# Kernel optimization log

Hardware: AMD Instinct MI355X
Metric: run time of the kernel (lower is better)

## Reference

```python
import jax, jax.numpy as jnp
import numpy as np

HEADS = 16
DIM_HEAD = 64
SCALE = DIM_HEAD ** -0.5
NEG = -jnp.finfo(jnp.float32).max


def setup_inputs() -> dict:
    key = jax.random.key(0)
    ks = jax.random.split(key, 5)
    b, n, dim = 2, 2048, 1024
    inner = HEADS * DIM_HEAD
    s = dim ** -0.5  # keep pre-softmax logits well-scaled
    return {
        "x": jax.random.normal(ks[0], (b, n, dim), jnp.float32),
        "mask": jnp.ones((b, n), dtype=bool),
        "Wq": jax.random.normal(ks[1], (dim, inner), jnp.float32) * s,
        "Wk": jax.random.normal(ks[2], (dim, inner), jnp.float32) * s,
        "Wv": jax.random.normal(ks[3], (dim, inner), jnp.float32) * s,
        "Wo": jax.random.normal(ks[4], (inner, dim), jnp.float32) * s,
    }


def reference(x, mask, Wq, Wk, Wv, Wo):
    b, n, _ = x.shape
    # projections, split heads: b n (h d) -> b h n d
    def split(t):
        return t.reshape(b, n, HEADS, DIM_HEAD).transpose(0, 2, 1, 3)
    q = split(x @ Wq)
    k = split(x @ Wk)
    v = split(x @ Wv)
    dots = jnp.einsum("bhid,bhjd->bhij", q, k) * SCALE  # [b,h,n,n]
    # padding mask: b j -> b 1 1 j
    dots = jnp.where(mask[:, None, None, :], dots, NEG)
    # causal mask (strict upper triangle masked)
    causal = jnp.triu(jnp.ones((n, n), dtype=bool), k=1)
    dots = jnp.where(causal, NEG, dots)
    attn = jax.nn.softmax(dots, axis=-1)
    out = jnp.einsum("bhij,bhjd->bhid", attn, v)
    out = out.transpose(0, 2, 1, 3).reshape(b, n, HEADS * DIM_HEAD)
    return out @ Wo
```

## Files before the change

kernel.cpp:

```cpp
#include <hip/hip_runtime.h>
#include <hip/hip_bf16.h>

typedef __bf16 bf16x8 __attribute__((ext_vector_type(8)));
typedef float f32x4 __attribute__((ext_vector_type(4)));
typedef unsigned short u16;
typedef unsigned int u32;

#define MFMA16(A, B, C) __builtin_amdgcn_mfma_f32_16x16x32_bf16((A), (B), (C), 0, 0, 0)

#define BATCH 2
#define SEQ   2048
#define DIM   1024
#define NHEAD 16
#define DHEAD 64
#define MROWS 4096
#define Q_SCALE 0.18033688f

__device__ __forceinline__ u16 f2bf(float f) {
    unsigned int u = __float_as_uint(f);
    u += 0x7fff + ((u >> 16) & 1);
    return (u16)(u >> 16);
}

__device__ __forceinline__ u32 pk2bf(float a, float b) {
    __hip_bfloat162 c = __float22bfloat162_rn(float2{a, b});
    u32 r;
    __builtin_memcpy(&r, &c, 4);
    return r;
}

__device__ __forceinline__ void glds16(const u16* g, u16* l) {
    __builtin_amdgcn_global_load_lds(
        (const __attribute__((address_space(1))) u32*)g,
        (__attribute__((address_space(3))) u32*)l, 16, 0, 0);
}

__global__ __launch_bounds__(256) void prep(const float* __restrict__ x,
                                            const float* __restrict__ wq,
                                            const float* __restrict__ wk,
                                            const float* __restrict__ wv,
                                            const float* __restrict__ wo,
                                            u16* __restrict__ xb,
                                            u16* __restrict__ wt) {
    const int b = blockIdx.x;
    const int t = threadIdx.x;
    if (b < 2048) {
        int i = (b * 256 + t) * 8;
        float4 a = *(const float4*)(x + i);
        float4 c = *(const float4*)(x + i + 4);
        u16 o[8] = {f2bf(a.x), f2bf(a.y), f2bf(a.z), f2bf(a.w),
                    f2bf(c.x), f2bf(c.y), f2bf(c.z), f2bf(c.w)};
        *(uint4*)(xb + i) = *(uint4*)o;
        return;
    }
    __shared__ u16 tile[64][65];
    const int bb = b - 2048;
    const int z = bb >> 8, rem = bb & 255;
    const float* W = (z == 0) ? wq : (z == 1) ? wk : (z == 2) ? wv : wo;
    u16* out = wt + (size_t)z * DIM * DIM;
    int k0 = (rem & 15) * 64;
    int n0 = (rem >> 4) * 64;
    int c = t & 63, r4 = t >> 6;
#pragma unroll
    for (int i = 0; i < 16; i++) {
        int row = i * 4 + r4;
        tile[row][c] = f2bf(W[(size_t)(k0 + row) * DIM + n0 + c]);
    }
    __syncthreads();
#pragma unroll
    for (int i = 0; i < 16; i++) {
        int row = i * 4 + r4;
        out[(size_t)(n0 + row) * DIM + k0 + c] = tile[c][row];
    }
}

__global__ __launch_bounds__(256) void gemm_qkv(const u16* __restrict__ xb,
                                                const u16* __restrict__ wt,
                                                u16* __restrict__ qb,
                                                u16* __restrict__ kb,
                                                u16* __restrict__ vtb) {
    __shared__ __align__(16) u16 SMEM[17408];
    u16* const As = SMEM;
    u16* const Bs = SMEM + 8192;

    const int z = blockIdx.z;
    const u16* Apan = xb;
    const u16* Bpan = wt + (size_t)z * DIM * DIM;
    const int m0 = blockIdx.y * 128, n0 = blockIdx.x * 128;
    const int t = threadIdx.x, w = t >> 6, lane = t & 63;
    const int quad = lane >> 4, l16 = lane & 15;
    const int wm = (w >> 1) * 64, wn = (w & 1) * 64;
    const int srow = lane >> 3;
    const int scol = ((lane & 7) ^ srow) * 8;
    const int fo0 = ((quad) ^ (l16 & 7)) * 8;
    const int fo1 = ((4 + quad) ^ (l16 & 7)) * 8;

    f32x4 acc[4][4] = {};
    for (int k0 = 0; k0 < DIM; k0 += 64) {
        if (k0) __syncthreads();
#pragma unroll
        for (int j = 0; j < 4; j++) {
            int rb = w * 32 + j * 8;
            glds16(Apan + (size_t)(m0 + rb + srow) * DIM + k0 + scol, &As[rb * 64]);
            glds16(Bpan + (size_t)(n0 + rb + srow) * DIM + k0 + scol, &Bs[rb * 64]);
        }
        __syncthreads();

        bf16x8 af[4][2], bfr[4][2];
#pragma unroll
        for (int mt = 0; mt < 4; mt++) {
            const u16* p = &As[(wm + mt * 16 + l16) * 64];
            af[mt][0] = *(const bf16x8*)(p + fo0);
            af[mt][1] = *(const bf16x8*)(p + fo1);
        }
#pragma unroll
        for (int nt = 0; nt < 4; nt++) {
            const u16* p = &Bs[(wn + nt * 16 + l16) * 64];
            bfr[nt][0] = *(const bf16x8*)(p + fo0);
            bfr[nt][1] = *(const bf16x8*)(p + fo1);
        }
#pragma unroll
        for (int mt = 0; mt < 4; mt++)
#pragma unroll
            for (int nt = 0; nt < 4; nt++) {
                acc[mt][nt] = MFMA16(af[mt][0], bfr[nt][0], acc[mt][nt]);
                acc[mt][nt] = MFMA16(af[mt][1], bfr[nt][1], acc[mt][nt]);
            }
    }

    const int bi = m0 >> 11;
    if (z < 2) {
        const float sc = (z == 0) ? Q_SCALE : 1.0f;
        u16* dst = (z == 0) ? qb : kb;
#pragma unroll
        for (int mt = 0; mt < 4; mt++)
#pragma unroll
            for (int nt = 0; nt < 4; nt++)
#pragma unroll
                for (int r = 0; r < 4; r++) {
                    int gm = m0 + wm + mt * 16 + quad * 4 + r;
                    int gc = n0 + wn + nt * 16 + l16;
                    int si = gm & (SEQ - 1);
                    int h = gc >> 6, d = gc & 63;
                    dst[(((size_t)bi * NHEAD + h) * SEQ + si) * DHEAD + d] =
                        f2bf(acc[mt][nt][r] * sc);
                }
    } else {
        __syncthreads();
        u16* T = SMEM;
#pragma unroll
        for (int mt = 0; mt < 4; mt++)
#pragma unroll
            for (int nt = 0; nt < 4; nt++)
#pragma unroll
                for (int r = 0; r < 4; r++)
                    T[(wn + nt * 16 + l16) * 136 + wm + mt * 16 + quad * 4 + r] =
                        f2bf(acc[mt][nt][r]);
        __syncthreads();
        const int row = t >> 1;
        const int half = (t & 1) * 64;
        const int gc = n0 + row;
        const int h = gc >> 6, d = gc & 63;
        const size_t gb = (((size_t)bi * NHEAD + h) * DHEAD + d) * SEQ +
                          (m0 & (SEQ - 1)) + half;
#pragma unroll
        for (int i = 0; i < 8; i++)
            *(uint4*)&vtb[gb + i * 8] = *(const uint4*)&T[row * 136 + half + i * 8];
    }
}

#define LPAD 72
#define OSTR 68
__global__ __launch_bounds__(256) void attn(const u16* __restrict__ qg,
                                            const u16* __restrict__ kg,
                                            const u16* __restrict__ vtg,
                                            u16* __restrict__ og) {
    __shared__ __align__(16) u16 Ks[2][64 * LPAD];
    __shared__ __align__(16) u16 Vs[2][64 * LPAD];
    __shared__ __align__(16) u16 Ps[64 * LPAD];
    __shared__ __align__(16) float Os[64 * OSTR];
    __shared__ float Ls[64];

    const int linear = blockIdx.x;
    const int kidx = linear >> 3;
    const int bh = (linear & 7) * 4 + (kidx >> 4);
    const int px = kidx & 15;
    const int t = threadIdx.x, w = t >> 6, lane = t & 63;
    const int quad = lane >> 4, l16 = lane & 15;
    const int wq32 = (w >> 1) * 32, kh = w & 1, kh32 = kh * 32;
    const int srow = t >> 2, sc16 = (t & 3) * 16;
    const size_t qkbase = (size_t)bh * SEQ;
    const size_t vbase = (size_t)bh * DHEAD;
    const int bi = bh >> 4, hh = bh & 15;

    uint4 pk0, pk1, pv0, pv1;
    auto prefetch = [&](int j0) {
        const u16* kp = &kg[(qkbase + j0 + srow) * DHEAD + sc16];
        pk0 = *(const uint4*)kp;
        pk1 = *(const uint4*)(kp + 8);
        const u16* vp = &vtg[(vbase + srow) * SEQ + j0 + sc16];
        pv0 = *(const uint4*)vp;
        pv1 = *(const uint4*)(vp + 8);
    };

    for (int half = 0; half < 2; half++) {
        const int qt = half ? (31 - px) : px;
        const int q0 = qt * 64;
        const int last = qt;
        const int rowmin = q0 + wq32;

        bf16x8 bq[2][2];
#pragma unroll
        for (int ct = 0; ct < 2; ct++) {
            const u16* qp = qg + (qkbase + q0 + wq32 + ct * 16 + l16) * DHEAD;
            bq[ct][0] = *(const bf16x8*)(qp + quad * 8);
            bq[ct][1] = *(const bf16x8*)(qp + 32 + quad * 8);
        }

        f32x4 accO[4][2] = {};
        float l_part[2] = {0.f, 0.f};

        prefetch(0);
        __syncthreads();

        for (int jt = 0; jt <= last; jt++) {
            const int buf = jt & 1;
            u16* ksb = &Ks[buf][0];
            u16* vsb = &Vs[buf][0];
            *(uint4*)&ksb[srow * LPAD + sc16] = pk0;
            *(uint4*)&ksb[srow * LPAD + sc16 + 8] = pk1;
            *(uint4*)&vsb[srow * LPAD + sc16] = pv0;
            *(uint4*)&vsb[srow * LPAD + sc16 + 8] = pv1;
            __syncthreads();
            if (jt < last) prefetch((jt + 1) * 64);

            const int j0 = jt * 64;
            if (j0 + kh32 > rowmin + 31) continue;
            const bool need_mask = (j0 + kh32 + 31 > rowmin);

            bf16x8 ak[2][2];
#pragma unroll
            for (int nt = 0; nt < 2; nt++) {
                const u16* kr = &ksb[(kh32 + nt * 16 + l16) * LPAD];
                ak[nt][0] = *(const bf16x8*)(kr + quad * 8);
                ak[nt][1] = *(const bf16x8*)(kr + 32 + quad * 8);
            }
            f32x4 s[2][2];
            __builtin_amdgcn_s_setprio(1);
#pragma unroll
            for (int nt = 0; nt < 2; nt++)
#pragma unroll
                for (int ct = 0; ct < 2; ct++) {
                    f32x4 aa = {};
                    aa = MFMA16(ak[nt][0], bq[ct][0], aa);
                    aa = MFMA16(ak[nt][1], bq[ct][1], aa);
                    s[nt][ct] = aa;
                }
            __builtin_amdgcn_s_setprio(0);

            if (need_mask) {
#pragma unroll
                for (int ct = 0; ct < 2; ct++) {
                    int qv = q0 + wq32 + ct * 16 + l16;
#pragma unroll
                    for (int nt = 0; nt < 2; nt++) {
                        int kb = j0 + kh32 + nt * 16 + quad * 4;
                        float p[4];
#pragma unroll
                        for (int r = 0; r < 4; r++)
                            p[r] = (kb + r > qv) ? 0.f
                                 : __builtin_amdgcn_exp2f(s[nt][ct][r]);
                        l_part[ct] += (p[0] + p[1]) + (p[2] + p[3]);
                        uint2 pkd = {pk2bf(p[0], p[1]), pk2bf(p[2], p[3])};
                        *(uint2*)&Ps[(wq32 + ct * 16 + l16) * LPAD + kh32 +
                                     nt * 16 + quad * 4] = pkd;
                    }
                }
            } else {
#pragma unroll
                for (int ct = 0; ct < 2; ct++)
#pragma unroll
                    for (int nt = 0; nt < 2; nt++) {
                        float p[4];
#pragma unroll
                        for (int r = 0; r < 4; r++)
                            p[r] = __builtin_amdgcn_exp2f(s[nt][ct][r]);
                        l_part[ct] += (p[0] + p[1]) + (p[2] + p[3]);
                        uint2 pkd = {pk2bf(p[0], p[1]), pk2bf(p[2], p[3])};
                        *(uint2*)&Ps[(wq32 + ct * 16 + l16) * LPAD + kh32 +
                                     nt * 16 + quad * 4] = pkd;
                    }
            }

            bf16x8 bp[2];
#pragma unroll
            for (int ct = 0; ct < 2; ct++)
                bp[ct] = *(const bf16x8*)&Ps[(wq32 + ct * 16 + l16) * LPAD +
                                             kh32 + quad * 8];
            __builtin_amdgcn_s_setprio(1);
#pragma unroll
            for (int mt = 0; mt < 4; mt++) {
                bf16x8 av = *(const bf16x8*)&vsb[(mt * 16 + l16) * LPAD +
                                                 kh32 + quad * 8];
#pragma unroll
                for (int ct = 0; ct < 2; ct++)
                    accO[mt][ct] = MFMA16(av, bp[ct], accO[mt][ct]);
            }
            __builtin_amdgcn_s_setprio(0);
        }

        float l2[2];
#pragma unroll
        for (int ct = 0; ct < 2; ct++) {
            float l = l_part[ct];
            l += __shfl_xor(l, 16);
            l += __shfl_xor(l, 32);
            l2[ct] = l;
        }
        if (kh == 1) {
            if (quad == 0) {
                Ls[wq32 + l16] = l2[0];
                Ls[wq32 + 16 + l16] = l2[1];
            }
#pragma unroll
            for (int mt = 0; mt < 4; mt++)
#pragma unroll
                for (int ct = 0; ct < 2; ct++)
                    *(float4*)&Os[(wq32 + ct * 16 + l16) * OSTR + mt * 16 +
                                  quad * 4] =
                        float4{accO[mt][ct][0], accO[mt][ct][1],
                               accO[mt][ct][2], accO[mt][ct][3]};
        }
        __syncthreads();
        if (kh == 0) {
#pragma unroll
            for (int ct = 0; ct < 2; ct++) {
                int q = q0 + wq32 + ct * 16 + l16;
                float rl = 1.0f / (l2[ct] + Ls[wq32 + ct * 16 + l16]);
                size_t obase = ((size_t)bi * SEQ + q) * DIM + hh * DHEAD;
#pragma unroll
                for (int mt = 0; mt < 4; mt++) {
                    float4 o = *(float4*)&Os[(wq32 + ct * 16 + l16) * OSTR +
                                             mt * 16 + quad * 4];
                    float v0 = (accO[mt][ct][0] + o.x) * rl;
                    float v1 = (accO[mt][ct][1] + o.y) * rl;
                    float v2 = (accO[mt][ct][2] + o.z) * rl;
                    float v3 = (accO[mt][ct][3] + o.w) * rl;
                    uint2 pkd = {pk2bf(v0, v1), pk2bf(v2, v3)};
                    *(uint2*)&og[obase + mt * 16 + quad * 4] = pkd;
                }
            }
        }
    }
}

__global__ __launch_bounds__(256) void gemm_out(const u16* __restrict__ ob,
                                                const u16* __restrict__ wot,
                                                float* __restrict__ out) {
    __shared__ __align__(16) u16 As[64 * 64];
    __shared__ __align__(16) u16 Bs[128 * 64];
    const int m0 = blockIdx.y * 64, n0 = blockIdx.x * 128;
    const int t = threadIdx.x, w = t >> 6, lane = t & 63;
    const int quad = lane >> 4, l16 = lane & 15;
    const int wm = (w >> 1) * 32, wn = (w & 1) * 64;
    const int srow = lane >> 3;
    const int scol = ((lane & 7) ^ srow) * 8;
    const int fo0 = ((quad) ^ (l16 & 7)) * 8;
    const int fo1 = ((4 + quad) ^ (l16 & 7)) * 8;

    f32x4 acc[2][4] = {};
    for (int k0 = 0; k0 < DIM; k0 += 64) {
        if (k0) __syncthreads();
#pragma unroll
        for (int j = 0; j < 2; j++) {
            int rb = w * 16 + j * 8;
            glds16(&ob[(size_t)(m0 + rb + srow) * DIM + k0 + scol], &As[rb * 64]);
        }
#pragma unroll
        for (int j = 0; j < 4; j++) {
            int rb = w * 32 + j * 8;
            glds16(&wot[(size_t)(n0 + rb + srow) * DIM + k0 + scol], &Bs[rb * 64]);
        }
        __syncthreads();

        bf16x8 af[2][2], bfr[4][2];
#pragma unroll
        for (int mt = 0; mt < 2; mt++) {
            const u16* p = &As[(wm + mt * 16 + l16) * 64];
            af[mt][0] = *(const bf16x8*)(p + fo0);
            af[mt][1] = *(const bf16x8*)(p + fo1);
        }
#pragma unroll
        for (int nt = 0; nt < 4; nt++) {
            const u16* p = &Bs[(wn + nt * 16 + l16) * 64];
            bfr[nt][0] = *(const bf16x8*)(p + fo0);
            bfr[nt][1] = *(const bf16x8*)(p + fo1);
        }
#pragma unroll
        for (int mt = 0; mt < 2; mt++)
#pragma unroll
            for (int nt = 0; nt < 4; nt++) {
                acc[mt][nt] = MFMA16(af[mt][0], bfr[nt][0], acc[mt][nt]);
                acc[mt][nt] = MFMA16(af[mt][1], bfr[nt][1], acc[mt][nt]);
            }
    }
#pragma unroll
    for (int mt = 0; mt < 2; mt++)
#pragma unroll
        for (int nt = 0; nt < 4; nt++)
#pragma unroll
            for (int r = 0; r < 4; r++) {
                int gm = m0 + wm + mt * 16 + quad * 4 + r;
                int gc = n0 + wn + nt * 16 + l16;
                out[(size_t)gm * DIM + gc] = acc[mt][nt][r];
            }
}

extern "C" void kernel_launch(void* const* d_in, const int* in_sizes, int n_in,
                              void* d_out, int out_size, void* d_ws, size_t ws_size,
                              hipStream_t stream) {
    const float* x  = (const float*)d_in[0];
    const float* wq = (const float*)d_in[2];
    const float* wk = (const float*)d_in[3];
    const float* wv = (const float*)d_in[4];
    const float* wo = (const float*)d_in[5];
    float* out = (float*)d_out;

    char* ws = (char*)d_ws;
    u16* xb  = (u16*)(ws);
    u16* wt  = (u16*)(ws + (8ull  << 20));
    u16* qb  = (u16*)(ws + (16ull << 20));
    u16* kb  = (u16*)(ws + (24ull << 20));
    u16* vtb = (u16*)(ws + (32ull << 20));
    u16* obf = (u16*)(ws + (40ull << 20));

    prep<<<3072, 256, 0, stream>>>(x, wq, wk, wv, wo, xb, wt);
    gemm_qkv<<<dim3(DIM / 128, MROWS / 128, 3), 256, 0, stream>>>(xb, wt, qb, kb, vtb);
    attn<<<512, 256, 0, stream>>>(qb, kb, vtb, obf);
    gemm_out<<<dim3(DIM / 128, MROWS / 64), 256, 0, stream>>>(
        obf, wt + 3ull * DIM * DIM, out);
}
```

Baseline: 166.0 us.

## Stage attention K/V via async global-to-LDS loads with XOR swizzle; enlarge out-GEMM tile

The attention kernel now loads K and V tiles straight into shared memory with the glds16 global-to-LDS path and an XOR-swizzled unpadded layout, replacing the register prefetch followed by explicit LDS stores. The swizzle is meant to keep the LDS fragment reads conflict-free without row padding. Separately, the output projection GEMM tile grows from 64x128 to 128x128, so each block does more MFMA work per staged tile, with half as many blocks and more accumulator registers per thread. The async staging into the alternate buffer must be correctly ordered by the existing barrier, and the larger GEMM tile may lower occupancy.

```diff
diff --git a/kernel.cpp b/kernel.cpp
--- a/kernel.cpp
+++ b/kernel.cpp
@@ -169,15 +169,15 @@
     }
 }
 
-#define LPAD 72
+#define PSTR 72
 #define OSTR 68
 __global__ __launch_bounds__(256) void attn(const u16* __restrict__ qg,
                                             const u16* __restrict__ kg,
                                             const u16* __restrict__ vtg,
                                             u16* __restrict__ og) {
-    __shared__ __align__(16) u16 Ks[2][64 * LPAD];
-    __shared__ __align__(16) u16 Vs[2][64 * LPAD];
-    __shared__ __align__(16) u16 Ps[64 * LPAD];
+    __shared__ __align__(16) u16 Ks[2][64 * 64];
+    __shared__ __align__(16) u16 Vs[2][64 * 64];
+    __shared__ __align__(16) u16 Ps[64 * PSTR];
     __shared__ __align__(16) float Os[64 * OSTR];
     __shared__ float Ls[64];
 
@@ -188,20 +188,26 @@
     const int t = threadIdx.x, w = t >> 6, lane = t & 63;
     const int quad = lane >> 4, l16 = lane & 15;
     const int wq32 = (w >> 1) * 32, kh = w & 1, kh32 = kh * 32;
-    const int srow = t >> 2, sc16 = (t & 3) * 16;
     const size_t qkbase = (size_t)bh * SEQ;
     const size_t vbase = (size_t)bh * DHEAD;
     const int bi = bh >> 4, hh = bh & 15;
 
-    uint4 pk0, pk1, pv0, pv1;
-    auto prefetch = [&](int j0) {
-        const u16* kp = &kg[(qkbase + j0 + srow) * DHEAD + sc16];
-        pk0 = *(const uint4*)kp;
-        pk1 = *(const uint4*)(kp + 8);
-        const u16* vp = &vtg[(vbase + srow) * SEQ + j0 + sc16];
-        pv0 = *(const uint4*)vp;
-        pv1 = *(const uint4*)(vp + 8);
+    const int sr8 = lane >> 3;
+    const int sg = ((lane & 7) ^ sr8) * 8;
+    auto stageKV = [&](int j0, int buf) {
+        u16* kd = &Ks[buf][0];
+        u16* vd = &Vs[buf][0];
+#pragma unroll
+        for (int i = 0; i < 2; i++) {
+            int rb = w * 16 + i * 8;
+            glds16(&kg[(qkbase + j0 + rb + sr8) * DHEAD + sg], &kd[rb * 64]);
+            glds16(&vtg[(vbase + rb + sr8) * SEQ + j0 + sg], &vd[rb * 64]);
+        }
     };
+
+    const int fo0 = ((quad) ^ (l16 & 7)) * 8;
+    const int fo1 = ((4 + quad) ^ (l16 & 7)) * 8;
+    const int vo = (((kh << 2) + quad) ^ (l16 & 7)) * 8;
 
     for (int half = 0; half < 2; half++) {
         const int qt = half ? (31 - px) : px;
@@ -220,30 +226,26 @@
         f32x4 accO[4][2] = {};
         float l_part[2] = {0.f, 0.f};
 
-        prefetch(0);
-        __syncthreads();
+        __syncthreads();
+        stageKV(0, 0);
 
         for (int jt = 0; jt <= last; jt++) {
             const int buf = jt & 1;
-            u16* ksb = &Ks[buf][0];
-            u16* vsb = &Vs[buf][0];
-            *(uint4*)&ksb[srow * LPAD + sc16] = pk0;
-            *(uint4*)&ksb[srow * LPAD + sc16 + 8] = pk1;
-            *(uint4*)&vsb[srow * LPAD + sc16] = pv0;
-            *(uint4*)&vsb[srow * LPAD + sc16 + 8] = pv1;
             __syncthreads();
-            if (jt < last) prefetch((jt + 1) * 64);
+            if (jt < last) stageKV((jt + 1) * 64, buf ^ 1);
 
             const int j0 = jt * 64;
             if (j0 + kh32 > rowmin + 31) continue;
             const bool need_mask = (j0 + kh32 + 31 > rowmin);
+            u16* ksb = &Ks[buf][0];
+            u16* vsb = &Vs[buf][0];
 
             bf16x8 ak[2][2];
 #pragma unroll
             for (int nt = 0; nt < 2; nt++) {
-                const u16* kr = &ksb[(kh32 + nt * 16 + l16) * LPAD];
-                ak[nt][0] = *(const bf16x8*)(kr + quad * 8);
-                ak[nt][1] = *(const bf16x8*)(kr + 32 + quad * 8);
+                const u16* kr = &ksb[(kh32 + nt * 16 + l16) * 64];
+                ak[nt][0] = *(const bf16x8*)(kr + fo0);
+                ak[nt][1] = *(const bf16x8*)(kr + fo1);
             }
             f32x4 s[2][2];
             __builtin_amdgcn_s_setprio(1);
@@ -272,7 +274,7 @@
                                  : __builtin_amdgcn_exp2f(s[nt][ct][r]);
                         l_part[ct] += (p[0] + p[1]) + (p[2] + p[3]);
                         uint2 pkd = {pk2bf(p[0], p[1]), pk2bf(p[2], p[3])};
-                        *(uint2*)&Ps[(wq32 + ct * 16 + l16) * LPAD + kh32 +
+                        *(uint2*)&Ps[(wq32 + ct * 16 + l16) * PSTR + kh32 +
                                      nt * 16 + quad * 4] = pkd;
                     }
                 }
@@ -287,7 +289,7 @@
                             p[r] = __builtin_amdgcn_exp2f(s[nt][ct][r]);
                         l_part[ct] += (p[0] + p[1]) + (p[2] + p[3]);
                         uint2 pkd = {pk2bf(p[0], p[1]), pk2bf(p[2], p[3])};
-                        *(uint2*)&Ps[(wq32 + ct * 16 + l16) * LPAD + kh32 +
+                        *(uint2*)&Ps[(wq32 + ct * 16 + l16) * PSTR + kh32 +
                                      nt * 16 + quad * 4] = pkd;
                     }
             }
@@ -295,13 +297,12 @@
             bf16x8 bp[2];
 #pragma unroll
             for (int ct = 0; ct < 2; ct++)
-                bp[ct] = *(const bf16x8*)&Ps[(wq32 + ct * 16 + l16) * LPAD +
+                bp[ct] = *(const bf16x8*)&Ps[(wq32 + ct * 16 + l16) * PSTR +
                                              kh32 + quad * 8];
             __builtin_amdgcn_s_setprio(1);
 #pragma unroll
             for (int mt = 0; mt < 4; mt++) {
-                bf16x8 av = *(const bf16x8*)&vsb[(mt * 16 + l16) * LPAD +
-                                                 kh32 + quad * 8];
+                bf16x8 av = *(const bf16x8*)&vsb[(mt * 16 + l16) * 64 + vo];
 #pragma unroll
                 for (int ct = 0; ct < 2; ct++)
                     accO[mt][ct] = MFMA16(av, bp[ct], accO[mt][ct]);
@@ -357,35 +358,31 @@
 __global__ __launch_bounds__(256) void gemm_out(const u16* __restrict__ ob,
                                                 const u16* __restrict__ wot,
                                                 float* __restrict__ out) {
-    __shared__ __align__(16) u16 As[64 * 64];
+    __shared__ __align__(16) u16 As[128 * 64];
     __shared__ __align__(16) u16 Bs[128 * 64];
-    const int m0 = blockIdx.y * 64, n0 = blockIdx.x * 128;
+    const int m0 = blockIdx.y * 128, n0 = blockIdx.x * 128;
     const int t = threadIdx.x, w = t >> 6, lane = t & 63;
     const int quad = lane >> 4, l16 = lane & 15;
-    const int wm = (w >> 1) * 32, wn = (w & 1) * 64;
+    const int wm = (w >> 1) * 64, wn = (w & 1) * 64;
     const int srow = lane >> 3;
     const int scol = ((lane & 7) ^ srow) * 8;
     const int fo0 = ((quad) ^ (l16 & 7)) * 8;
     const int fo1 = ((4 + quad) ^ (l16 & 7)) * 8;
 
-    f32x4 acc[2][4] = {};
+    f32x4 acc[4][4] = {};
     for (int k0 = 0; k0 < DIM; k0 += 64) {
         if (k0) __syncthreads();
 #pragma unroll
-        for (int j = 0; j < 2; j++) {
-            int rb = w * 16 + j * 8;
-            glds16(&ob[(size_t)(m0 + rb + srow) * DIM + k0 + scol], &As[rb * 64]);
-        }
-#pragma unroll
         for (int j = 0; j < 4; j++) {
             int rb = w * 32 + j * 8;
+            glds16(&ob[(size_t)(m0 + rb + srow) * DIM + k0 + scol], &As[rb * 64]);
             glds16(&wot[(size_t)(n0 + rb + srow) * DIM + k0 + scol], &Bs[rb * 64]);
         }
         __syncthreads();
 
-        bf16x8 af[2][2], bfr[4][2];
-#pragma unroll
-        for (int mt = 0; mt < 2; mt++) {
+        bf16x8 af[4][2], bfr[4][2];
+#pragma unroll
+        for (int mt = 0; mt < 4; mt++) {
             const u16* p = &As[(wm + mt * 16 + l16) * 64];
             af[mt][0] = *(const bf16x8*)(p + fo0);
             af[mt][1] = *(const bf16x8*)(p + fo1);
@@ -397,7 +394,7 @@
             bfr[nt][1] = *(const bf16x8*)(p + fo1);
         }
 #pragma unroll
-        for (int mt = 0; mt < 2; mt++)
+        for (int mt = 0; mt < 4; mt++)
 #pragma unroll
             for (int nt = 0; nt < 4; nt++) {
                 acc[mt][nt] = MFMA16(af[mt][0], bfr[nt][0], acc[mt][nt]);
@@ -405,7 +402,7 @@
             }
     }
 #pragma unroll
-    for (int mt = 0; mt < 2; mt++)
+    for (int mt = 0; mt < 4; mt++)
 #pragma unroll
         for (int nt = 0; nt < 4; nt++)
 #pragma unroll
@@ -437,6 +434,6 @@
     prep<<<3072, 256, 0, stream>>>(x, wq, wk, wv, wo, xb, wt);
     gemm_qkv<<<dim3(DIM / 128, MROWS / 128, 3), 256, 0, stream>>>(xb, wt, qb, kb, vtb);
     attn<<<512, 256, 0, stream>>>(qb, kb, vtb, obf);
-    gemm_out<<<dim3(DIM / 128, MROWS / 64), 256, 0, stream>>>(
+    gemm_out<<<dim3(DIM / 128, MROWS / 128), 256, 0, stream>>>(
         obf, wt + 3ull * DIM * DIM, out);
 }
```

After: 175.4 us. 5.7% more time.
